# Kernel optimization log

Hardware: AMD Instinct MI355X
Metric: run time of the kernel (lower is better)

The kernel has to match this reference:

```python
import jax, jax.numpy as jnp
import numpy as np

MARGIN = 0.1          # cfg.\u03b1
NUM_CLASSES = 1000    # number of distinct labels
N, D = 1_000_000, 128


def setup_inputs() -> dict:
    key = jax.random.key(0)
    k1, k2, k3 = jax.random.split(key, 3)
    feat1 = jax.random.normal(k1, (N, D), dtype=jnp.float32)
    feat2 = jax.random.normal(k2, (N, D), dtype=jnp.float32)
    label1 = jax.random.randint(k3, (N,), 0, NUM_CLASSES, dtype=jnp.int64)
    return {"feat1": feat1, "feat2": feat2, "label1": label1}


def _l2_normalize(x):
    # Normalize(power=2): x / (sum(x^2, dim=1, keepdim=True))^(1/2)
    norm = jnp.sqrt(jnp.sum(x * x, axis=1, keepdims=True))
    return x / norm


def reference(feat1, feat2, label1):
    f1 = _l2_normalize(feat1)
    f2 = _l2_normalize(feat2)
    # Per-class mean pooling (segment mean), vectorized over all classes.
    counts = jax.ops.segment_sum(jnp.ones((f1.shape[0],), f1.dtype), label1,
                                 num_segments=NUM_CLASSES)              # [C]
    s1 = jax.ops.segment_sum(f1, label1, num_segments=NUM_CLASSES)      # [C, D]
    s2 = jax.ops.segment_sum(f2, label1, num_segments=NUM_CLASSES)      # [C, D]
    denom = jnp.maximum(counts, 1.0)[:, None]
    c1 = s1 / denom
    c2 = s2 / denom
    # MSELoss(reduction='sum') per class center pair, hinged at margin.
    per_class = jnp.sum((c1 - c2) ** 2, axis=1)                         # [C]
    hinge = jnp.maximum(per_class - MARGIN, 0.0)
    # Classes absent from label1 contribute nothing (matches unique() loop).
    hinge = jnp.where(counts > 0, hinge, 0.0)
    return jnp.sum(hinge)
```

## Files before the change

### kernel.cpp

```cpp
#include <hip/hip_runtime.h>

#define NUM_C 1000
#define DIM 128
#define MARGIN 0.1f


__global__ void k_init(unsigned* __restrict__ counts, float* __restrict__ out, int out_n) {
    int t = threadIdx.x;
    for (int i = t; i < 1024; i += blockDim.x) counts[i] = 0u;
    if (t < out_n) out[t] = 0.0f;
}

__global__ void k_hist(const int* __restrict__ label, unsigned* __restrict__ counts, int n) {
    __shared__ unsigned h[NUM_C];
    for (int i = threadIdx.x; i < NUM_C; i += blockDim.x) h[i] = 0u;
    __syncthreads();
    int idx = blockIdx.x * blockDim.x + threadIdx.x;
    int stride = gridDim.x * blockDim.x;
    for (int i = idx; i < n; i += stride) atomicAdd(&h[label[i]], 1u);
    __syncthreads();
    for (int i = threadIdx.x; i < NUM_C; i += blockDim.x) {
        unsigned v = h[i];
        if (v) atomicAdd(&counts[i], v);
    }
}

__global__ void k_scan(const unsigned* __restrict__ counts,
                       unsigned* __restrict__ offsets,
                       unsigned* __restrict__ cursor) {
    __shared__ unsigned s[1024];
    int t = threadIdx.x;
    unsigned v = (t < NUM_C) ? counts[t] : 0u;
    s[t] = v;
    __syncthreads();
    for (int off = 1; off < 1024; off <<= 1) {
        unsigned x = (t >= off) ? s[t - off] : 0u;
        __syncthreads();
        s[t] += x;
        __syncthreads();
    }
    if (t < NUM_C) {
        unsigned e = s[t] - v;
        offsets[t] = e;
        cursor[t] = e;
    }
}

__global__ void k_scatter(const int* __restrict__ label,
                          unsigned* __restrict__ cursor,
                          unsigned* __restrict__ perm, int n) {
    int idx = blockIdx.x * blockDim.x + threadIdx.x;
    int stride = gridDim.x * blockDim.x;
    for (int i = idx; i < n; i += stride) {
        int c = label[i];
        unsigned p = atomicAdd(&cursor[c], 1u);
        perm[p] = (unsigned)i;
    }
}

__launch_bounds__(256)
__global__ void k_main(const float* __restrict__ f1, const float* __restrict__ f2,
                       const unsigned* __restrict__ offsets,
                       const unsigned* __restrict__ counts,
                       const unsigned* __restrict__ perm,
                       float* __restrict__ out) {
    const int c = blockIdx.x;
    const unsigned start = offsets[c];
    const unsigned cnt = counts[c];
    const int wave = threadIdx.x >> 6;
    const int lane = threadIdx.x & 63;

    float a1x = 0.f, a1y = 0.f, a2x = 0.f, a2y = 0.f;

    auto body = [&](unsigned r) {
        unsigned row = perm[start + r];
        const float2* p1 = (const float2*)(f1 + (size_t)row * DIM);
        const float2* p2 = (const float2*)(f2 + (size_t)row * DIM);
        float2 v1 = p1[lane];
        float2 v2 = p2[lane];
        float s1 = v1.x * v1.x + v1.y * v1.y;
        float s2 = v2.x * v2.x + v2.y * v2.y;
        #pragma unroll
        for (int off = 32; off; off >>= 1) {
            s1 += __shfl_xor(s1, off);
            s2 += __shfl_xor(s2, off);
        }
        float i1 = 1.0f / sqrtf(s1);
        float i2 = 1.0f / sqrtf(s2);
        a1x += v1.x * i1; a1y += v1.y * i1;
        a2x += v2.x * i2; a2y += v2.y * i2;
    };

    unsigned r = (unsigned)wave;
    for (; r + 4 < cnt; r += 8) { body(r); body(r + 4); }
    for (; r < cnt; r += 4) { body(r); }

    __shared__ float lds1[4][DIM];
    __shared__ float lds2[4][DIM];
    lds1[wave][2 * lane]     = a1x;
    lds1[wave][2 * lane + 1] = a1y;
    lds2[wave][2 * lane]     = a2x;
    lds2[wave][2 * lane + 1] = a2y;
    __syncthreads();

    float sq = 0.f;
    if (threadIdx.x < DIM) {
        int d = threadIdx.x;
        float s1 = lds1[0][d] + lds1[1][d] + lds1[2][d] + lds1[3][d];
        float s2 = lds2[0][d] + lds2[1][d] + lds2[2][d] + lds2[3][d];
        float denom = fmaxf((float)cnt, 1.0f);
        float dif = (s1 - s2) / denom;
        sq = dif * dif;
    }
    #pragma unroll
    for (int off = 32; off; off >>= 1) sq += __shfl_xor(sq, off);

    __shared__ float partial[4];
    if (lane == 0) partial[wave] = sq;
    __syncthreads();
    if (threadIdx.x == 0) {
        float tot = partial[0] + partial[1];
        float h = tot - MARGIN;
        if (h > 0.f && cnt > 0u) atomicAdd(out, h);
    }
}

extern "C" void kernel_launch(void* const* d_in, const int* in_sizes, int n_in,
                              void* d_out, int out_size, void* d_ws, size_t ws_size,
                              hipStream_t stream) {
    const float* feat1 = (const float*)d_in[0];
    const float* feat2 = (const float*)d_in[1];
    const int* label = (const int*)d_in[2];
    const int n = in_sizes[2];

    char* ws = (char*)d_ws;
    unsigned* counts  = (unsigned*)(ws + 0);
    unsigned* offsets = (unsigned*)(ws + 4096);
    unsigned* cursor  = (unsigned*)(ws + 8192);
    unsigned* perm    = (unsigned*)(ws + 12288);
    float* out = (float*)d_out;

    k_init<<<1, 256, 0, stream>>>(counts, out, out_size);
    k_hist<<<256, 256, 0, stream>>>(label, counts, n);
    k_scan<<<1, 1024, 0, stream>>>(counts, offsets, cursor);
    k_scatter<<<256, 256, 0, stream>>>(label, cursor, perm, n);
    k_main<<<NUM_C, 256, 0, stream>>>(feat1, feat2, offsets, counts, perm, out);
}
```

Before: 1.199 ms.

## Split each class across multiple blocks with atomic diff accumulation and final kernel

Each class is now processed by SPLIT blocks instead of one, so more blocks run concurrently across the GPU's compute units. Each block accumulates the difference of normalized rows and atomically adds it into a per-class workspace buffer, and a new final kernel computes the hinge loss per class. Loads widen to float4, with each wave processing two rows at a time, one per half-wave. The cost is an extra kernel launch, a larger zero-init pass, and float atomics whose summation order is nondeterministic.

```diff
diff --git a/kernel.cpp b/kernel.cpp
--- a/kernel.cpp
+++ b/kernel.cpp
@@ -3,12 +3,16 @@
 #define NUM_C 1000
 #define DIM 128
 #define MARGIN 0.1f
+#define SPLIT 8
 
 
-__global__ void k_init(unsigned* __restrict__ counts, float* __restrict__ out, int out_n) {
-    int t = threadIdx.x;
-    for (int i = t; i < 1024; i += blockDim.x) counts[i] = 0u;
-    if (t < out_n) out[t] = 0.0f;
+__global__ void k_init(unsigned* __restrict__ counts, float* __restrict__ diffsum,
+                       float* __restrict__ out, int out_n) {
+    int idx = blockIdx.x * blockDim.x + threadIdx.x;
+    int stride = gridDim.x * blockDim.x;
+    if (idx < 1024) counts[idx] = 0u;
+    for (int i = idx; i < NUM_C * DIM; i += stride) diffsum[i] = 0.0f;
+    if (idx < out_n) out[idx] = 0.0f;
 }
 
 __global__ void k_hist(const int* __restrict__ label, unsigned* __restrict__ counts, int n) {
@@ -63,65 +67,83 @@
                        const unsigned* __restrict__ offsets,
                        const unsigned* __restrict__ counts,
                        const unsigned* __restrict__ perm,
-                       float* __restrict__ out) {
-    const int c = blockIdx.x;
+                       float* __restrict__ diffsum) {
+    const int c   = blockIdx.x / SPLIT;
+    const int sub = blockIdx.x % SPLIT;
     const unsigned start = offsets[c];
     const unsigned cnt = counts[c];
     const int wave = threadIdx.x >> 6;
     const int lane = threadIdx.x & 63;
+    const int g    = lane >> 5;
+    const int lg   = lane & 31;
+    const unsigned slot = (unsigned)(sub * 4 + wave);
 
-    float a1x = 0.f, a1y = 0.f, a2x = 0.f, a2y = 0.f;
+    float4 acc = make_float4(0.f, 0.f, 0.f, 0.f);
 
-    auto body = [&](unsigned r) {
-        unsigned row = perm[start + r];
-        const float2* p1 = (const float2*)(f1 + (size_t)row * DIM);
-        const float2* p2 = (const float2*)(f2 + (size_t)row * DIM);
-        float2 v1 = p1[lane];
-        float2 v2 = p2[lane];
-        float s1 = v1.x * v1.x + v1.y * v1.y;
-        float s2 = v2.x * v2.x + v2.y * v2.y;
+    auto body = [&](unsigned base) {
+        unsigned rr = base + (unsigned)g;
+        bool act = rr < cnt;
+        float4 v1 = make_float4(0.f, 0.f, 0.f, 0.f);
+        float4 v2 = make_float4(0.f, 0.f, 0.f, 0.f);
+        if (act) {
+            unsigned row = perm[start + rr];
+            const float4* p1 = (const float4*)(f1 + (size_t)row * DIM);
+            const float4* p2 = (const float4*)(f2 + (size_t)row * DIM);
+            v1 = p1[lg];
+            v2 = p2[lg];
+        }
+        float s1 = v1.x * v1.x + v1.y * v1.y + v1.z * v1.z + v1.w * v1.w;
+        float s2 = v2.x * v2.x + v2.y * v2.y + v2.z * v2.z + v2.w * v2.w;
         #pragma unroll
-        for (int off = 32; off; off >>= 1) {
+        for (int off = 16; off; off >>= 1) {
             s1 += __shfl_xor(s1, off);
             s2 += __shfl_xor(s2, off);
         }
-        float i1 = 1.0f / sqrtf(s1);
-        float i2 = 1.0f / sqrtf(s2);
-        a1x += v1.x * i1; a1y += v1.y * i1;
-        a2x += v2.x * i2; a2y += v2.y * i2;
+        float i1 = act ? (1.0f / sqrtf(s1)) : 0.0f;
+        float i2 = act ? (1.0f / sqrtf(s2)) : 0.0f;
+        acc.x += v1.x * i1 - v2.x * i2;
+        acc.y += v1.y * i1 - v2.y * i2;
+        acc.z += v1.z * i1 - v2.z * i2;
+        acc.w += v1.w * i1 - v2.w * i2;
     };
 
-    unsigned r = (unsigned)wave;
-    for (; r + 4 < cnt; r += 8) { body(r); body(r + 4); }
-    for (; r < cnt; r += 4) { body(r); }
+    for (unsigned base = 2u * slot; base < cnt; base += 128u) {
+        body(base);
+        body(base + 64u);
+    }
 
-    __shared__ float lds1[4][DIM];
-    __shared__ float lds2[4][DIM];
-    lds1[wave][2 * lane]     = a1x;
-    lds1[wave][2 * lane + 1] = a1y;
-    lds2[wave][2 * lane]     = a2x;
-    lds2[wave][2 * lane + 1] = a2y;
+    acc.x += __shfl_xor(acc.x, 32);
+    acc.y += __shfl_xor(acc.y, 32);
+    acc.z += __shfl_xor(acc.z, 32);
+    acc.w += __shfl_xor(acc.w, 32);
+
+    __shared__ float lds[4][DIM];
+    if (lane < 32) *(float4*)&lds[wave][lg * 4] = acc;
     __syncthreads();
 
-    float sq = 0.f;
-    if (threadIdx.x < DIM) {
-        int d = threadIdx.x;
-        float s1 = lds1[0][d] + lds1[1][d] + lds1[2][d] + lds1[3][d];
-        float s2 = lds2[0][d] + lds2[1][d] + lds2[2][d] + lds2[3][d];
-        float denom = fmaxf((float)cnt, 1.0f);
-        float dif = (s1 - s2) / denom;
-        sq = dif * dif;
+    int d = threadIdx.x;
+    if (d < DIM) {
+        float v = lds[0][d] + lds[1][d] + lds[2][d] + lds[3][d];
+        atomicAdd(&diffsum[c * DIM + d], v);
     }
+}
+
+__launch_bounds__(64)
+__global__ void k_final(const float* __restrict__ diffsum,
+                        const unsigned* __restrict__ counts,
+                        float* __restrict__ out) {
+    int c = blockIdx.x;
+    int lane = threadIdx.x;
+    unsigned cnt = counts[c];
+    float inv = 1.0f / fmaxf((float)cnt, 1.0f);
+    float x0 = diffsum[c * DIM + lane] * inv;
+    float x1 = diffsum[c * DIM + 64 + lane] * inv;
+    float sq = x0 * x0 + x1 * x1;
     #pragma unroll
     for (int off = 32; off; off >>= 1) sq += __shfl_xor(sq, off);
-
-    __shared__ float partial[4];
-    if (lane == 0) partial[wave] = sq;
-    __syncthreads();
-    if (threadIdx.x == 0) {
-        float tot = partial[0] + partial[1];
-        float h = tot - MARGIN;
-        if (h > 0.f && cnt > 0u) atomicAdd(out, h);
+    if (lane == 0 && cnt > 0u) {
+        float h = sq - MARGIN;
+        if (h > 0.0f) atomicAdd(out, h);
     }
 }
 
@@ -137,12 +159,14 @@
     unsigned* counts  = (unsigned*)(ws + 0);
     unsigned* offsets = (unsigned*)(ws + 4096);
     unsigned* cursor  = (unsigned*)(ws + 8192);
-    unsigned* perm    = (unsigned*)(ws + 12288);
+    float*    diffsum = (float*)(ws + 16384);
+    unsigned* perm    = (unsigned*)(ws + 532480);
     float* out = (float*)d_out;
 
-    k_init<<<1, 256, 0, stream>>>(counts, out, out_size);
+    k_init<<<64, 256, 0, stream>>>(counts, diffsum, out, out_size);
     k_hist<<<256, 256, 0, stream>>>(label, counts, n);
     k_scan<<<1, 1024, 0, stream>>>(counts, offsets, cursor);
     k_scatter<<<256, 256, 0, stream>>>(label, cursor, perm, n);
-    k_main<<<NUM_C, 256, 0, stream>>>(feat1, feat2, offsets, counts, perm, out);
+    k_main<<<NUM_C * SPLIT, 256, 0, stream>>>(feat1, feat2, offsets, counts, perm, diffsum);
+    k_final<<<NUM_C, 64, 0, stream>>>(diffsum, counts, out);
 }
```

New measurement: 1.159 ms. -3.3%, faster.
